# Optimization experiments

Measured on AMD Instinct MI355X. Metric: run time of the kernel, lower is better.

The kernel has to match this reference:

```python
import jax, jax.numpy as jnp
import numpy as np

C = 1024      # n_feature // 2
OUT = 128     # out_dim
B, T, F = 16, 512, 2048


def conv1d(x, w, b):
    # x: [B, C, T], w: [O, I, 3], padding=1 stride=1 (torch Conv1d semantics)
    y = jax.lax.conv_general_dilated(x, w, window_strides=(1,), padding=[(1, 1)],
                                     dimension_numbers=('NCH', 'OIH', 'NCH'))
    return y + b[None, :, None]


def setup_inputs() -> dict:
    key = jax.random.key(0)
    ks = jax.random.split(key, 20)
    s = 0.02
    inp = {
        'inputs': jax.random.normal(ks[0], (B, T, F), jnp.float32),
        'wq': jax.random.normal(ks[1], (C, C, 3), jnp.float32) * s,
        'bq': jnp.zeros((C,), jnp.float32),
        'wk': jax.random.normal(ks[2], (C, C, 3), jnp.float32) * s,
        'bk': jnp.zeros((C,), jnp.float32),
        'wv': jax.random.normal(ks[3], (C, C, 3), jnp.float32) * s,
        'bv': jnp.zeros((C,), jnp.float32),
        'gamma': jax.random.normal(ks[4], (), jnp.float32) * 0.5,
        'w_fcf': jax.random.normal(ks[5], (C, C), jnp.float32) * s,
        'b_fcf': jnp.zeros((C,), jnp.float32),
        'w_fc1f': jax.random.normal(ks[6], (OUT, C), jnp.float32) * s,
        'b_fc1f': jnp.zeros((OUT,), jnp.float32),
        'w_fcr': jax.random.normal(ks[7], (C, C), jnp.float32) * s,
        'b_fcr': jnp.zeros((C,), jnp.float32),
        'w_fc1r': jax.random.normal(ks[8], (OUT, C), jnp.float32) * s,
        'b_fc1r': jnp.zeros((OUT,), jnp.float32),
        'inputs_len': jax.random.randint(ks[9], (B,), 64, T, dtype=jnp.int32),
        'is_query': 1,
    }
    return inp


def reference(inputs, wq, bq, wk, bk, wv, bv, gamma,
              w_fcf, b_fcf, w_fc1f, b_fc1f, w_fcr, b_fcr, w_fc1r, b_fc1r,
              inputs_len, is_query):
    nby2 = inputs.shape[-1] // 2
    base_x_f = inputs[:, :, nby2:]
    base_x_r = inputs[:, :, :nby2]

    def ragged_self_att(x):
        # x: [B, T, C]; attention only over each sample's first q_len frames,
        # remaining frames passed through untouched (matches per-sample slicing).
        b, t, c = x.shape
        pos = jnp.arange(t)
        mask = pos[None, :] < inputs_len[:, None]            # [B, T]
        xm = x * mask[..., None]                              # zero beyond q_len => conv zero-pad semantics at boundary
        xc = jnp.transpose(xm, (0, 2, 1))                     # [B, C, T]
        q = jnp.transpose(conv1d(xc, wq, bq), (0, 2, 1))      # [B, T, C]
        k = conv1d(xc, wk, bk)                                # [B, C, T]
        v = conv1d(xc, wv, bv)                                # [B, C, T]
        scale = jnp.sqrt(inputs_len.astype(x.dtype))[:, None, None]  # sqrt(dep)=sqrt(q_len)
        scores = jnp.einsum('btc,bcs->bts', q, k) / scale     # [B, T, T]
        scores = jnp.where(mask[:, None, :], scores, -jnp.inf)
        attn = jax.nn.softmax(scores, axis=-1)
        out = jnp.einsum('bcs,bts->btc', v, attn)             # bmm(v, attn^T), transposed to [B,T,C]
        feat = gamma * out + xm
        return jnp.where(mask[..., None], feat, x)

    a_f = ragged_self_att(base_x_f)
    a_r = ragged_self_att(base_x_r)

    def head(x, w1, b1, w2, b2):
        h = jax.nn.relu(jnp.einsum('btc,oc->bto', x, w1) + b1)
        # dropout skipped (eval / deterministic reference)
        return jax.nn.relu(jnp.einsum('btc,oc->bto', h, w2) + b2)

    y_f = head(a_f, w_fcf, b_fcf, w_fc1f, b_fc1f)
    y_r = head(a_r, w_fcr, b_fcr, w_fc1r, b_fc1r)
    return jnp.concatenate([y_f, y_r], axis=-1)              # [B, T, 2*OUT]
```

## Files before the change

### kernel.cpp

```cpp
#include <hip/hip_runtime.h>
#include <hip/hip_bf16.h>

typedef unsigned short u16;
typedef __attribute__((ext_vector_type(8))) __bf16 bf16x8;
typedef __attribute__((ext_vector_type(4))) float f32x4;

__device__ __forceinline__ u16 f2b(float f) {
  __hip_bfloat16 h = __float2bfloat16(f);
  u16 u;
  __builtin_memcpy(&u, &h, 2);
  return u;
}

__device__ __forceinline__ void gload16(const void* g, void* l) {
  __builtin_amdgcn_global_load_lds(
      (const __attribute__((address_space(1))) unsigned int*)g,
      (__attribute__((address_space(3))) unsigned int*)l, 16, 0, 0);
}

__device__ __forceinline__ bf16x8 ldsF(const char* base, int row, int ch) {
  return *(const bf16x8*)(base + row * 64 + ((ch ^ ((row >> 1) & 3)) << 4));
}

struct G2 {
  const u16* A;
  const u16* Bt;
  const u16* Bt2;
  void* out;
  void* out2;
  void* out3;
  const float* bias;
  const float* bias2;
  const float* bias3;
  const u16* zpage;
  int K;
};

#define STG(kt, bi)                                                            \
  {                                                                            \
    _Pragma("unroll") for (int r_ = 0; r_ < 2; ++r_) {                         \
      const int idx_ = r_ * 512 + tid;                                         \
      const int row_ = idx_ >> 2;                                              \
      const int k_ = (kt) * 32 + (((idx_ & 3) ^ ((row_ >> 1) & 3)) << 3);      \
      const u16* src_;                                                         \
      if constexpr (TAG == 0) {                                                \
        const int gm_ = m0 + row_;                                             \
        const int t_ = (gm_ & 511) + (k_ >> 10) - 1;                           \
        src_ = ((unsigned)t_ < 512u)                                           \
                   ? p.A + ((((long)(gm_ >> 9) << 9) + t_) << 10) + (k_ & 1023)\
                   : p.zpage;                                                  \
      } else {                                                                 \
        src_ = p.A + (long)(m0 + row_) * 1024 + k_;                            \
      }                                                                        \
      gload16(src_, (char*)lds + (bi) * 32768 + r_ * 8192 + w * 1024);         \
    }                                                                          \
    _Pragma("unroll") for (int r_ = 0; r_ < 2; ++r_) {                         \
      const int idx_ = r_ * 512 + tid;                                         \
      const int row_ = idx_ >> 2;                                              \
      const int k_ = (kt) * 32 + (((idx_ & 3) ^ ((row_ >> 1) & 3)) << 3);      \
      const u16* src_ = Bb + (long)(n0 + row_) * LDB + k_;                     \
      gload16(src_, (char*)lds + (bi) * 32768 + 16384 + r_ * 8192 + w * 1024); \
    }                                                                          \
  }

#define CMP(bi)                                                                \
  {                                                                            \
    const char* Ab_ = (const char*)lds + (bi) * 32768;                         \
    bf16x8 aF[8], bF[4];                                                       \
    const int ch_ = lane >> 4;                                                 \
    const int rA_ = wr * 128 + (lane & 15);                                    \
    const int rB_ = wc * 64 + (lane & 15);                                     \
    _Pragma("unroll") for (int mi = 0; mi < 8; ++mi)                           \
        aF[mi] = ldsF(Ab_, rA_ + mi * 16, ch_);                                \
    _Pragma("unroll") for (int ni = 0; ni < 4; ++ni)                           \
        bF[ni] = ldsF(Ab_ + 16384, rB_ + ni * 16, ch_);                        \
    __builtin_amdgcn_s_setprio(1);                                             \
    _Pragma("unroll") for (int mi = 0; mi < 8; ++mi)                           \
        _Pragma("unroll") for (int ni = 0; ni < 4; ++ni)                       \
            acc[mi][ni] = __builtin_amdgcn_mfma_f32_16x16x32_bf16(             \
                aF[mi], bF[ni], acc[mi][ni], 0, 0, 0);                         \
    __builtin_amdgcn_s_setprio(0);                                             \
  }

template <int TAG>
__global__ __launch_bounds__(512, 2) void gemm256_k(G2 p) {
  __shared__ __align__(16) char lds[4 * 32768];

  constexpr int NTN = (TAG == 0) ? 12 : 4;
  constexpr int LDB = (TAG == 0) ? 3072 : 1024;

  const int tid = threadIdx.x;
  const int lane = tid & 63;
  const int w = tid >> 6;
  const int wr = w >> 2;
  const int wc = w & 3;

  const int cpx = gridDim.x >> 3;
  const int wg = (blockIdx.x & 7) * cpx + (blockIdx.x >> 3);
  const int n0 = (wg % NTN) * 256;
  const int m0 = (wg / NTN) * 256;

  const u16* Bb = (TAG == 1 && m0 >= 8192) ? p.Bt2 : p.Bt;

  const int NT = p.K >> 5;

  f32x4 acc[8][4] = {};

  STG(0, 0);
  STG(1, 1);
  STG(2, 2);
  asm volatile("s_waitcnt vmcnt(8)" ::: "memory");
  __builtin_amdgcn_s_barrier();

  int t = 0;
  for (; t < NT - 3; ++t) {
    STG(t + 3, (t + 3) & 3);
    CMP(t & 3);
    asm volatile("s_waitcnt vmcnt(8)" ::: "memory");
    __builtin_amdgcn_s_barrier();
  }
  CMP(t & 3);
  asm volatile("s_waitcnt vmcnt(4)" ::: "memory");
  __builtin_amdgcn_s_barrier();
  ++t;
  CMP(t & 3);
  asm volatile("s_waitcnt vmcnt(0)" ::: "memory");
  __builtin_amdgcn_s_barrier();
  ++t;
  CMP(t & 3);

  const int fr = (lane >> 4) * 4;
  const int fc = lane & 15;

  if constexpr (TAG == 0) {
    const int opid = n0 >> 10;
    const int nc = n0 & 1023;
    const float* bp = (opid == 0) ? p.bias : (opid == 1) ? p.bias2 : p.bias3;
    u16* qo = (u16*)p.out;
    u16* ko = (u16*)p.out2;
    u16* vo = (u16*)p.out3;
#pragma unroll
    for (int ni = 0; ni < 4; ++ni) {
      const int col = nc + wc * 64 + ni * 16 + fc;
      const float bsv = bp[col];
#pragma unroll
      for (int mi = 0; mi < 8; ++mi)
#pragma unroll
        for (int j = 0; j < 4; ++j) {
          const int grow = m0 + wr * 128 + mi * 16 + fr + j;
          const u16 v = f2b(acc[mi][ni][j] + bsv);
          if (opid == 0) qo[(long)grow * 1024 + col] = v;
          else if (opid == 1) ko[(long)grow * 1024 + col] = v;
          else vo[((long)(grow >> 9) * 1024 + col) * 512 + (grow & 511)] = v;
        }
    }
  } else {
    const float* bp = (m0 >> 13) ? p.bias2 : p.bias;
    u16* ho = (u16*)p.out;
#pragma unroll
    for (int ni = 0; ni < 4; ++ni) {
      const int col = n0 + wc * 64 + ni * 16 + fc;
      const float bsv = bp[col];
#pragma unroll
      for (int mi = 0; mi < 8; ++mi)
#pragma unroll
        for (int j = 0; j < 4; ++j) {
          const int grow = m0 + wr * 128 + mi * 16 + fr + j;
          ho[(long)grow * 1024 + col] = f2b(fmaxf(acc[mi][ni][j] + bsv, 0.f));
        }
    }
  }
}

enum { OP_SCORES = 2, OP_PV = 3, OP_HEAD2 = 5 };

struct GP {
  const u16* A;
  const u16* Bt;
  int lda, ldb, K;
  long sAz, sBz;
  void* out;
  const float* bias;
  const float* bias2;
  const float* gamma;
  const float* x_full;
  const int* lens;
};

template <int TAG>
__global__ __launch_bounds__(256, 4) void gemm_k(GP p) {
  __shared__ __align__(16) u16 As[128 * 64];
  __shared__ __align__(16) u16 Bs[128 * 64];

  const int tid = threadIdx.x;
  const int lane = tid & 63;
  const int w = tid >> 6;
  const int wr = (w >> 1) * 64;
  const int wc = (w & 1) * 64;
  const int m0 = blockIdx.y * 128;
  const int n0 = blockIdx.x * 128;
  const int z = blockIdx.z;

  const u16* Ab = p.A + (long)z * p.sAz;
  const u16* Bb = p.Bt + (long)z * p.sBz;

  const int sr = tid >> 3;
  const int scs = (((tid & 7) ^ ((tid >> 3) & 7)) << 3);

  f32x4 acc[4][4] = {};

  for (int k0 = 0; k0 < p.K; k0 += 64) {
#pragma unroll
    for (int R = 0; R < 4; ++R) {
      const int row = R * 32 + sr;
      const u16* srcA = Ab + (long)(m0 + row) * p.lda + (k0 + scs);
      gload16(srcA, (char*)As + R * 4096 + w * 1024);
      const u16* srcB = Bb + (long)(n0 + row) * p.ldb + (k0 + scs);
      gload16(srcB, (char*)Bs + R * 4096 + w * 1024);
    }
    __syncthreads();
#pragma unroll
    for (int kk = 0; kk < 64; kk += 32) {
      const int slot = (kk >> 3) + (lane >> 4);
      bf16x8 aF[4], bF[4];
#pragma unroll
      for (int mi = 0; mi < 4; ++mi) {
        const int r = wr + mi * 16 + (lane & 15);
        aF[mi] = *(const bf16x8*)(As + r * 64 + ((slot ^ (r & 7)) << 3));
      }
#pragma unroll
      for (int ni = 0; ni < 4; ++ni) {
        const int r = wc + ni * 16 + (lane & 15);
        bF[ni] = *(const bf16x8*)(Bs + r * 64 + ((slot ^ (r & 7)) << 3));
      }
#pragma unroll
      for (int mi = 0; mi < 4; ++mi)
#pragma unroll
        for (int ni = 0; ni < 4; ++ni)
          acc[mi][ni] = __builtin_amdgcn_mfma_f32_16x16x32_bf16(
              aF[mi], bF[ni], acc[mi][ni], 0, 0, 0);
    }
    __syncthreads();
  }

  const int fr = (lane >> 4) * 4;
  const int fc = lane & 15;

  if constexpr (TAG == OP_SCORES) {
    float* op = (float*)p.out + (long)z * 262144;
#pragma unroll
    for (int ni = 0; ni < 4; ++ni) {
      const int col = n0 + wc + ni * 16 + fc;
#pragma unroll
      for (int mi = 0; mi < 4; ++mi)
#pragma unroll
        for (int j = 0; j < 4; ++j) {
          const int row = m0 + wr + mi * 16 + fr + j;
          op[(long)row * 512 + col] = acc[mi][ni][j];
        }
    }
  } else if constexpr (TAG == OP_PV) {
    u16* op = (u16*)p.out;
    const int half = z >> 4, b = z & 15;
    const int len = p.lens[b];
    const float g = *p.gamma;
    const float* xb = p.x_full + ((long)b * 512) * 2048 + (half == 0 ? 1024 : 0);
#pragma unroll
    for (int ni = 0; ni < 4; ++ni) {
      const int col = n0 + wc + ni * 16 + fc;
#pragma unroll
      for (int mi = 0; mi < 4; ++mi)
#pragma unroll
        for (int j = 0; j < 4; ++j) {
          const int t = m0 + wr + mi * 16 + fr + j;
          const float xv = xb[(long)t * 2048 + col];
          const float r = (t < len) ? fmaf(g, acc[mi][ni][j], xv) : xv;
          op[((long)z * 512 + t) * 1024 + col] = f2b(r);
        }
    }
  } else {
    float* op = (float*)p.out;
    const float* bp = (z == 0) ? p.bias : p.bias2;
#pragma unroll
    for (int ni = 0; ni < 4; ++ni) {
      const int col = wc + ni * 16 + fc;
      const float bsv = bp[col];
#pragma unroll
      for (int mi = 0; mi < 4; ++mi)
#pragma unroll
        for (int j = 0; j < 4; ++j) {
          const int row = m0 + wr + mi * 16 + fr + j;
          op[(long)row * 256 + z * 128 + col] = fmaxf(acc[mi][ni][j] + bsv, 0.f);
        }
    }
  }
}

__global__ __launch_bounds__(256) void softmax_k(const float* scores, u16* attn,
                                                 const int* lens) {
  const int row = blockIdx.x * 4 + (threadIdx.x >> 6);
  const int lane = threadIdx.x & 63;
  const int len = lens[(row >> 9) & 15];
  const float inv = rsqrtf((float)len);
  const float* sr = scores + (long)row * 512;
  u16* ar = attn + (long)row * 512;
  float e[8];
  float mx = -1e30f;
#pragma unroll
  for (int j = 0; j < 8; ++j) {
    const int s = j * 64 + lane;
    const float v = (s < len) ? sr[s] * inv : -1e30f;
    e[j] = v;
    mx = fmaxf(mx, v);
  }
#pragma unroll
  for (int d = 1; d < 64; d <<= 1) mx = fmaxf(mx, __shfl_xor(mx, d));
  float sum = 0.f;
#pragma unroll
  for (int j = 0; j < 8; ++j) {
    const int s = j * 64 + lane;
    const float t = (s < len) ? __expf(e[j] - mx) : 0.f;
    e[j] = t;
    sum += t;
  }
#pragma unroll
  for (int d = 1; d < 64; d <<= 1) sum += __shfl_xor(sum, d);
  const float r = 1.f / sum;
#pragma unroll
  for (int j = 0; j < 8; ++j) ar[j * 64 + lane] = f2b(e[j] * r);
}

__global__ void convw_k(const float* wsrc, u16* wt) {
  const int idx = blockIdx.x * 256 + threadIdx.x;
  const float* s = wsrc + (long)idx * 3;
  u16* d = wt + (long)(idx >> 10) * 3072 + (idx & 1023);
  d[0] = f2b(s[0]);
  d[1024] = f2b(s[1]);
  d[2048] = f2b(s[2]);
}

__global__ void castk(const float* s, u16* d, int n) {
  const int i = blockIdx.x * 256 + threadIdx.x;
  if (i < n) d[i] = f2b(s[i]);
}

__global__ void xmk(const float* inputs, u16* xm, const int* lens) {
  const int idx = blockIdx.x * 256 + threadIdx.x;
  const int row = idx >> 8;
  const int c4 = (idx & 255) * 4;
  const int xoff = (row & 8192) ? 0 : 1024;
  const bool live = (row & 511) < lens[(row >> 9) & 15];
  float4 v = {0.f, 0.f, 0.f, 0.f};
  if (live) v = *(const float4*)(inputs + (long)(row & 8191) * 2048 + xoff + c4);
  ushort4 o;
  o.x = f2b(v.x); o.y = f2b(v.y); o.z = f2b(v.z); o.w = f2b(v.w);
  *(ushort4*)(xm + (long)row * 1024 + c4) = o;
}

__global__ void zerok(u16* p) { p[blockIdx.x * 256 + threadIdx.x] = 0; }

extern "C" void kernel_launch(void* const* d_in, const int* in_sizes, int n_in,
                              void* d_out, int out_size, void* d_ws, size_t ws_size,
                              hipStream_t stream) {
  const float* inputs = (const float*)d_in[0];
  const float* wq = (const float*)d_in[1];
  const float* bq = (const float*)d_in[2];
  const float* wk = (const float*)d_in[3];
  const float* bk = (const float*)d_in[4];
  const float* wv = (const float*)d_in[5];
  const float* bv = (const float*)d_in[6];
  const float* gamma = (const float*)d_in[7];
  const float* w_fcf = (const float*)d_in[8];
  const float* b_fcf = (const float*)d_in[9];
  const float* w_fc1f = (const float*)d_in[10];
  const float* b_fc1f = (const float*)d_in[11];
  const float* w_fcr = (const float*)d_in[12];
  const float* b_fcr = (const float*)d_in[13];
  const float* w_fc1r = (const float*)d_in[14];
  const float* b_fc1r = (const float*)d_in[15];
  const int* lens = (const int*)d_in[16];
  float* out = (float*)d_out;

  char* ws = (char*)d_ws;
  size_t off = 0;
  auto alloc = [&](size_t n) {
    char* p = ws + off;
    off += (n + 255) & ~(size_t)255;
    return p;
  };

  u16* wt_all = (u16*)alloc(3072l * 3072 * 2);
  u16* zpage = (u16*)alloc(4096);
  u16* xm = (u16*)alloc(16384l * 1024 * 2);
  u16* qb = (u16*)alloc(16384l * 1024 * 2);
  u16* kb = (u16*)alloc(16384l * 1024 * 2);
  u16* vb = (u16*)alloc(32l * 1024 * 512 * 2);
  u16* attn = wt_all;
  float* scores = (float*)xm;
  u16* w1b = (u16*)xm;
  u16* w2b = w1b + 2l * 1024 * 1024;
  u16* abuf = qb;
  u16* hbuf = kb;

  zerok<<<8, 256, 0, stream>>>(zpage);
  convw_k<<<4096, 256, 0, stream>>>(wq, wt_all);
  convw_k<<<4096, 256, 0, stream>>>(wk, wt_all + 1024l * 3072);
  convw_k<<<4096, 256, 0, stream>>>(wv, wt_all + 2048l * 3072);
  xmk<<<16384, 256, 0, stream>>>(inputs, xm, lens);

  {
    G2 g{};
    g.A = xm; g.Bt = wt_all; g.zpage = zpage; g.K = 3072;
    g.out = qb; g.out2 = kb; g.out3 = vb;
    g.bias = bq; g.bias2 = bk; g.bias3 = bv;
    gemm256_k<0><<<768, 512, 0, stream>>>(g);
  }

  {
    GP g{};
    g.A = qb; g.Bt = kb; g.lda = 1024; g.ldb = 1024; g.K = 1024;
    g.sAz = 512l * 1024; g.sBz = 512l * 1024; g.out = scores;
    gemm_k<OP_SCORES><<<dim3(4, 4, 32), 256, 0, stream>>>(g);
  }
  softmax_k<<<4096, 256, 0, stream>>>(scores, attn, lens);

  castk<<<4096, 256, 0, stream>>>(w_fcf, w1b, 1024 * 1024);
  castk<<<4096, 256, 0, stream>>>(w_fcr, w1b + 1024l * 1024, 1024 * 1024);
  castk<<<512, 256, 0, stream>>>(w_fc1f, w2b, 128 * 1024);
  castk<<<512, 256, 0, stream>>>(w_fc1r, w2b + 128l * 1024, 128 * 1024);

  {
    GP g{};
    g.A = attn; g.Bt = vb; g.lda = 512; g.ldb = 512; g.K = 512;
    g.sAz = 512l * 512; g.sBz = 1024l * 512;
    g.out = abuf; g.gamma = gamma; g.x_full = inputs; g.lens = lens;
    gemm_k<OP_PV><<<dim3(8, 4, 32), 256, 0, stream>>>(g);
  }

  {
    G2 h{};
    h.A = abuf; h.Bt = w1b; h.Bt2 = w1b + 1024l * 1024; h.K = 1024;
    h.out = hbuf; h.bias = b_fcf; h.bias2 = b_fcr;
    gemm256_k<1><<<256, 512, 0, stream>>>(h);
  }

  {
    GP g{};
    g.A = hbuf; g.Bt = w2b; g.lda = 1024; g.ldb = 1024; g.K = 1024;
    g.sAz = 8192l * 1024; g.sBz = 128l * 1024;
    g.out = out; g.bias = b_fc1f; g.bias2 = b_fc1r;
    gemm_k<OP_HEAD2><<<dim3(1, 64, 2), 256, 0, stream>>>(g);
  }
}
```

Baseline: 678.5 us.

## Split GEMM main loop into two phases interleaving loads with MFMA

The main K-loop body is split into two half-phases, each computing half of the M-fragments. The A-tile and B-tile global-to-LDS loads are issued separately, one per phase, with barriers and priority hints arranged so one wave group's memory traffic overlaps another's MFMA work. This is a ping-pong style schedule meant to hide load and LDS latency and cut per-phase register pressure, at the cost of two extra barriers per iteration.

Measured after the change: 690.7 us. Within noise of the previous version (+1.8%).

```diff
diff --git a/kernel.cpp b/kernel.cpp
--- a/kernel.cpp
+++ b/kernel.cpp
@@ -36,7 +36,7 @@
   int K;
 };
 
-#define STG(kt, bi)                                                            \
+#define STG_A(kt, bi)                                                          \
   {                                                                            \
     _Pragma("unroll") for (int r_ = 0; r_ < 2; ++r_) {                         \
       const int idx_ = r_ * 512 + tid;                                         \
@@ -54,6 +54,10 @@
       }                                                                        \
       gload16(src_, (char*)lds + (bi) * 32768 + r_ * 8192 + w * 1024);         \
     }                                                                          \
+  }
+
+#define STG_B(kt, bi)                                                          \
+  {                                                                            \
     _Pragma("unroll") for (int r_ = 0; r_ < 2; ++r_) {                         \
       const int idx_ = r_ * 512 + tid;                                         \
       const int row_ = idx_ >> 2;                                              \
@@ -63,22 +67,68 @@
     }                                                                          \
   }
 
+#define PH_A(bi, STAGE_CODE)                                                   \
+  {                                                                            \
+    const char* Ab_ = (const char*)lds + (bi) * 32768;                         \
+    const int ch_ = lane >> 4;                                                 \
+    const int rA_ = wr * 128 + (lane & 15);                                    \
+    const int rB_ = wc * 64 + (lane & 15);                                     \
+    bf16x8 aF[4];                                                              \
+    _Pragma("unroll") for (int mi = 0; mi < 4; ++mi)                           \
+        aF[mi] = ldsF(Ab_, rA_ + mi * 16, ch_);                                \
+    _Pragma("unroll") for (int ni = 0; ni < 4; ++ni)                           \
+        bF[ni] = ldsF(Ab_ + 16384, rB_ + ni * 16, ch_);                        \
+    STAGE_CODE                                                                 \
+    __builtin_amdgcn_s_barrier();                                              \
+    asm volatile("s_waitcnt lgkmcnt(0)" ::: "memory");                         \
+    __builtin_amdgcn_sched_barrier(0);                                         \
+    __builtin_amdgcn_s_setprio(1);                                             \
+    _Pragma("unroll") for (int mi = 0; mi < 4; ++mi)                           \
+        _Pragma("unroll") for (int ni = 0; ni < 4; ++ni)                       \
+            acc[mi][ni] = __builtin_amdgcn_mfma_f32_16x16x32_bf16(             \
+                aF[mi], bF[ni], acc[mi][ni], 0, 0, 0);                         \
+    __builtin_amdgcn_s_setprio(0);                                             \
+    __builtin_amdgcn_s_barrier();                                              \
+  }
+
+#define PH_B(bi, STAGE_CODE, VMW)                                              \
+  {                                                                            \
+    const char* Ab_ = (const char*)lds + (bi) * 32768;                         \
+    const int ch_ = lane >> 4;                                                 \
+    const int rA_ = wr * 128 + (lane & 15);                                    \
+    bf16x8 aF[4];                                                              \
+    _Pragma("unroll") for (int mi = 0; mi < 4; ++mi)                           \
+        aF[mi] = ldsF(Ab_, rA_ + 64 + mi * 16, ch_);                           \
+    STAGE_CODE                                                                 \
+    __builtin_amdgcn_s_barrier();                                              \
+    asm volatile("s_waitcnt lgkmcnt(0)" ::: "memory");                         \
+    __builtin_amdgcn_sched_barrier(0);                                         \
+    __builtin_amdgcn_s_setprio(1);                                             \
+    _Pragma("unroll") for (int mi = 0; mi < 4; ++mi)                           \
+        _Pragma("unroll") for (int ni = 0; ni < 4; ++ni)                       \
+            acc[4 + mi][ni] = __builtin_amdgcn_mfma_f32_16x16x32_bf16(         \
+                aF[mi], bF[ni], acc[4 + mi][ni], 0, 0, 0);                     \
+    __builtin_amdgcn_s_setprio(0);                                             \
+    VMW                                                                        \
+    __builtin_amdgcn_s_barrier();                                              \
+  }
+
 #define CMP(bi)                                                                \
   {                                                                            \
     const char* Ab_ = (const char*)lds + (bi) * 32768;                         \
-    bf16x8 aF[8], bF[4];                                                       \
+    bf16x8 aF[8], bF2[4];                                                      \
     const int ch_ = lane >> 4;                                                 \
     const int rA_ = wr * 128 + (lane & 15);                                    \
     const int rB_ = wc * 64 + (lane & 15);                                     \
     _Pragma("unroll") for (int mi = 0; mi < 8; ++mi)                           \
         aF[mi] = ldsF(Ab_, rA_ + mi * 16, ch_);                                \
     _Pragma("unroll") for (int ni = 0; ni < 4; ++ni)                           \
-        bF[ni] = ldsF(Ab_ + 16384, rB_ + ni * 16, ch_);                        \
+        bF2[ni] = ldsF(Ab_ + 16384, rB_ + ni * 16, ch_);                       \
     __builtin_amdgcn_s_setprio(1);                                             \
     _Pragma("unroll") for (int mi = 0; mi < 8; ++mi)                           \
         _Pragma("unroll") for (int ni = 0; ni < 4; ++ni)                       \
             acc[mi][ni] = __builtin_amdgcn_mfma_f32_16x16x32_bf16(             \
-                aF[mi], bF[ni], acc[mi][ni], 0, 0, 0);                         \
+                aF[mi], bF2[ni], acc[mi][ni], 0, 0, 0);                        \
     __builtin_amdgcn_s_setprio(0);                                             \
   }
 
@@ -106,18 +156,20 @@
 
   f32x4 acc[8][4] = {};
 
-  STG(0, 0);
-  STG(1, 1);
-  STG(2, 2);
+  STG_A(0, 0); STG_B(0, 0);
+  STG_A(1, 1); STG_B(1, 1);
+  STG_A(2, 2); STG_B(2, 2);
   asm volatile("s_waitcnt vmcnt(8)" ::: "memory");
   __builtin_amdgcn_s_barrier();
 
   int t = 0;
   for (; t < NT - 3; ++t) {
-    STG(t + 3, (t + 3) & 3);
-    CMP(t & 3);
-    asm volatile("s_waitcnt vmcnt(8)" ::: "memory");
-    __builtin_amdgcn_s_barrier();
+    const int bi = t & 3;
+    const int b3 = (t + 3) & 3;
+    bf16x8 bF[4];
+    PH_A(bi, { STG_A(t + 3, b3); });
+    PH_B(bi, { STG_B(t + 3, b3); },
+         { asm volatile("s_waitcnt vmcnt(8)" ::: "memory"); });
   }
   CMP(t & 3);
   asm volatile("s_waitcnt vmcnt(4)" ::: "memory");
```
